# Performance work log

Measured on AMD Instinct MI355X. Metric: run time of the kernel, lower is better.

## Reference

```python
import jax, jax.numpy as jnp
import numpy as np

D_MODEL = 1024
N_HEADS = 16
HEAD_DIM = D_MODEL // N_HEADS


def setup_inputs() -> dict:
    key = jax.random.key(0)
    k1, k2, k3 = jax.random.split(key, 3)
    B, T = 4, 2048
    x = jax.random.normal(k1, (B, T, D_MODEL), dtype=jnp.float32)
    # match nn.Linear default init scale roughly (small weights for stability)
    w_qkv = jax.random.normal(k2, (D_MODEL, 3 * D_MODEL), dtype=jnp.float32) / np.sqrt(D_MODEL)
    w_proj = jax.random.normal(k3, (D_MODEL, D_MODEL), dtype=jnp.float32) / np.sqrt(D_MODEL)
    b_proj = jnp.zeros((D_MODEL,), dtype=jnp.float32)
    return {"x": x, "w_qkv": w_qkv, "w_proj": w_proj, "b_proj": b_proj}


def reference(x, w_qkv, w_proj, b_proj):
    B, T, C = x.shape
    qkv = x @ w_qkv  # [B,T,3C]
    q, k, v = jnp.split(qkv, 3, axis=-1)
    # [B, H, T, hd]
    q = q.reshape(B, T, N_HEADS, HEAD_DIM).transpose(0, 2, 1, 3)
    k = k.reshape(B, T, N_HEADS, HEAD_DIM).transpose(0, 2, 1, 3)
    v = v.reshape(B, T, N_HEADS, HEAD_DIM).transpose(0, 2, 1, 3)
    scale = 1.0 / np.sqrt(HEAD_DIM).astype(np.float32)
    att = jnp.einsum("bhqd,bhkd->bhqk", q, k) * scale
    causal = jnp.tril(jnp.ones((T, T), dtype=bool))
    att = jnp.where(causal[None, None], att, jnp.float32(-jnp.inf))
    att = jax.nn.softmax(att, axis=-1)
    # dropout p=0.0 (eval) -> identity
    out = jnp.einsum("bhqk,bhkd->bhqd", att, v)
    out = out.transpose(0, 2, 1, 3).reshape(B, T, C)
    return out @ w_proj + b_proj
```

## Files before the change

kernel.cpp:

```cpp
#include <hip/hip_runtime.h>
#include <stdint.h>

#define D_MODEL 1024
#define N_HEADS 16
#define HEAD_DIM 64
#define BATCH 4
#define SEQ 2048
#define ROWS (BATCH * SEQ)
#define K3 (3 * D_MODEL)
#define NQT (SEQ / 64)
#define SCALE_Q 0.1803368867f

typedef unsigned short u16;
typedef unsigned int u32;
typedef __attribute__((ext_vector_type(8))) short short8;
typedef __attribute__((ext_vector_type(4))) float floatx4;

typedef const __attribute__((address_space(1))) u32* gptr_t;
typedef __attribute__((address_space(3))) u32* lptr_t;

__device__ __forceinline__ unsigned cvt_pk(float lo, float hi) {
    unsigned r;
    asm("v_cvt_pk_bf16_f32 %0, %1, %2" : "=v"(r) : "v"(lo), "v"(hi));
    return r;
}

__global__ __launch_bounds__(256) void conv_f2b4(const float* __restrict__ x,
                                                 u16* __restrict__ xb, int n4) {
    int i = blockIdx.x * 256 + threadIdx.x;
    if (i < n4) {
        float4 v = ((const float4*)x)[i];
        uint2 p;
        p.x = cvt_pk(v.x, v.y);
        p.y = cvt_pk(v.z, v.w);
        ((uint2*)xb)[i] = p;
    }
}

__global__ __launch_bounds__(256) void transpose_f2b_t(const float* __restrict__ w,
                                                       u16* __restrict__ wt,
                                                       int R, int C) {
    __shared__ u16 tile[64][65];
    const int tx = threadIdx.x & 63;
    const int ty = threadIdx.x >> 6;
    const int r0 = blockIdx.y * 64, c0 = blockIdx.x * 64;
    #pragma unroll
    for (int i = 0; i < 16; i += 2) {
        const float a = w[(size_t)(r0 + i * 4 + ty) * C + c0 + tx];
        const float b = w[(size_t)(r0 + (i + 1) * 4 + ty) * C + c0 + tx];
        const unsigned p = cvt_pk(a, b);
        tile[i * 4 + ty][tx] = (u16)p;
        tile[(i + 1) * 4 + ty][tx] = (u16)(p >> 16);
    }
    __syncthreads();
    #pragma unroll
    for (int i = 0; i < 16; ++i) {
        const int c = i * 4 + ty;
        wt[(size_t)(c0 + c) * R + r0 + tx] = tile[tx][c];
    }
}

__global__ __launch_bounds__(256) void transpose_v2(const u16* __restrict__ v,
                                                    u16* __restrict__ vt) {
    __shared__ u16 tile[64][65];
    const int bh = blockIdx.y;
    const int t0 = blockIdx.x * 64;
    const int tx = threadIdx.x & 63, ty = threadIdx.x >> 6;
    const u16* src = v + ((size_t)bh * SEQ + t0) * HEAD_DIM;
    #pragma unroll
    for (int i = 0; i < 16; ++i) {
        const int r = i * 4 + ty;
        tile[r][tx] = src[r * HEAD_DIM + tx];
    }
    __syncthreads();
    u16* dst = vt + (size_t)bh * HEAD_DIM * SEQ + t0;
    #pragma unroll
    for (int i = 0; i < 16; ++i) {
        const int d = i * 4 + ty;
        dst[(size_t)d * SEQ + tx] = tile[tx][d];
    }
}

#define GEMM_CORE_GLD(KDIM, NXB)                                               \
    __shared__ u16 As[128][64];                                                \
    __shared__ u16 Bs[128][64];                                                \
    const int tid  = threadIdx.x;                                              \
    const int wave = tid >> 6, lane = tid & 63;                                \
    const int quad = lane >> 4, l15 = lane & 15;                               \
    const int wr = wave >> 1, wc = wave & 1;                                   \
    const int bid = (int)(blockIdx.y * gridDim.x + blockIdx.x);                \
    const int nwg = (int)(gridDim.x * gridDim.y);                              \
    const int swz = (bid & 7) * (nwg >> 3) + (bid >> 3);      \
    const int m0 = (swz / (NXB)) * 128, n0 = (swz % (NXB)) * 128;              \
    const int lrow8 = lane >> 3;                                               \
    const int csw = 8 * ((lane & 7) ^ lrow8);           \
    const int swA = (l15 & 7) * 8;                      \
    floatx4 acc[4][4] = {};                                                    \
    for (int k0 = 0; k0 < (KDIM); k0 += 64) {                                  \
        _Pragma("unroll")                                                      \
        for (int i = 0; i < 4; ++i) {                                          \
            const int rb = i * 32 + wave * 8;                                  \
            const int r  = rb + lrow8;                                         \
            __builtin_amdgcn_global_load_lds(                                  \
                (gptr_t)(A + (size_t)(m0 + r) * (KDIM) + k0 + csw),            \
                (lptr_t)(&As[rb][0]), 16, 0, 0);                               \
            __builtin_amdgcn_global_load_lds(                                  \
                (gptr_t)(Bt + (size_t)(n0 + r) * (KDIM) + k0 + csw),           \
                (lptr_t)(&Bs[rb][0]), 16, 0, 0);                               \
        }                                                                      \
        __syncthreads();                                                       \
        _Pragma("unroll")                                                      \
        for (int ks = 0; ks < 2; ++ks) {                                       \
            const int kk = ks * 32 + quad * 8;                                 \
            short8 af[4], bf[4];                                               \
            _Pragma("unroll")                                                  \
            for (int t = 0; t < 4; ++t) {                                      \
                af[t] = *(const short8*)&As[wr * 64 + t * 16 + l15][kk ^ swA]; \
                bf[t] = *(const short8*)&Bs[wc * 64 + t * 16 + l15][kk ^ swA]; \
            }                                                                  \
            _Pragma("unroll")                                                  \
            for (int i = 0; i < 4; ++i)                                        \
                _Pragma("unroll")                                              \
                for (int j = 0; j < 4; ++j)                                    \
                    acc[i][j] = __builtin_amdgcn_mfma_f32_16x16x32_bf16(       \
                        af[i], bf[j], acc[i][j], 0, 0, 0);                     \
        }                                                                      \
        __syncthreads();                                                       \
    }

__global__ __launch_bounds__(256) void gemm_qkv(const u16* __restrict__ A,
                                                const u16* __restrict__ Bt,
                                                u16* __restrict__ qo,
                                                u16* __restrict__ ko,
                                                u16* __restrict__ vo) {
    GEMM_CORE_GLD(D_MODEL, 24)
    const int which = n0 >> 10;
    u16* dst = which == 0 ? qo : (which == 1 ? ko : vo);
    const float scl = which == 0 ? SCALE_Q : 1.f;
    #pragma unroll
    for (int i = 0; i < 4; ++i)
        #pragma unroll
        for (int j = 0; j < 4; ++j) {
            const int col = n0 + wc * 64 + j * 16 + l15;
            const int rb  = m0 + wr * 64 + i * 16 + quad * 4;
            const int cc  = col & 1023;
            const int h = cc >> 6, d = cc & 63;
            #pragma unroll
            for (int rr = 0; rr < 4; rr += 2) {
                const unsigned pw = cvt_pk(acc[i][j][rr] * scl,
                                           acc[i][j][rr + 1] * scl);
                int row = rb + rr;
                int b_ = row >> 11, t_ = row & 2047;
                dst[(((size_t)(b_ * N_HEADS + h)) * SEQ + t_) * HEAD_DIM + d] =
                    (u16)pw;
                row = rb + rr + 1;
                b_ = row >> 11; t_ = row & 2047;
                dst[(((size_t)(b_ * N_HEADS + h)) * SEQ + t_) * HEAD_DIM + d] =
                    (u16)(pw >> 16);
            }
        }
}

__global__ __launch_bounds__(256) void gemm_proj(const u16* __restrict__ A,
                                                 const u16* __restrict__ Bt,
                                                 const float* __restrict__ bias,
                                                 float* __restrict__ out) {
    GEMM_CORE_GLD(D_MODEL, 8)
    #pragma unroll
    for (int i = 0; i < 4; ++i)
        #pragma unroll
        for (int j = 0; j < 4; ++j) {
            const int col = n0 + wc * 64 + j * 16 + l15;
            const int rb  = m0 + wr * 64 + i * 16 + quad * 4;
            const float bv = bias[col];
            #pragma unroll
            for (int rr = 0; rr < 4; ++rr) {
                const int row = rb + rr;
                out[(size_t)row * D_MODEL + col] = acc[i][j][rr] + bv;
            }
        }
}

__global__ __launch_bounds__(256, 4) void attn_mfma(const u16* __restrict__ q,
                                                    const u16* __restrict__ k,
                                                    const u16* __restrict__ vt,
                                                    u16* __restrict__ o) {
    __shared__ u16 Ks[2][64][64];
    __shared__ u16 Vs[2][64][64];
    __shared__ u16 Plds[4][16][64];
    const int tid = threadIdx.x;
    const int w = tid >> 6, lane = tid & 63;
    const int quad = lane >> 4, l15 = lane & 15;
    const int bid = (int)(blockIdx.y * 16 + blockIdx.x);
    const int swzb = (bid & 7) * 128 + (bid >> 3);
    const int bh = swzb >> 4;
    const int qx = swzb & 15;
    const int b = bh >> 4, h = bh & 15;
    const u16* kb  = k  + (size_t)bh * SEQ * HEAD_DIM;
    const u16* vtb = vt + (size_t)bh * HEAD_DIM * SEQ;
    const int lrow8 = lane >> 3;
    const int csw = 8 * ((lane & 7) ^ lrow8);
    const int swA = (l15 & 7) * 8;
    const int r0 = w * 16 + lrow8;
    const short8 ones = {0x3F80, 0x3F80, 0x3F80, 0x3F80,
                         0x3F80, 0x3F80, 0x3F80, 0x3F80};

    #pragma unroll 1
    for (int seg = 0; seg < 2; ++seg) {
        const int qt = seg ? qx : (NQT - 1 - qx);
        const int qrow = qt * 64 + w * 16 + l15;
        const u16* qp = q + ((size_t)bh * SEQ + qrow) * HEAD_DIM + quad * 8;
        const short8 bq0 = *(const short8*)(qp);
        const short8 bq1 = *(const short8*)(qp + 32);

        floatx4 O[4] = {};
        floatx4 Lacc = {};

        __syncthreads();
        __builtin_amdgcn_global_load_lds(
            (gptr_t)(kb + (size_t)(r0) * HEAD_DIM + csw),
            (lptr_t)(&Ks[0][w * 16][0]), 16, 0, 0);
        __builtin_amdgcn_global_load_lds(
            (gptr_t)(kb + (size_t)(r0 + 8) * HEAD_DIM + csw),
            (lptr_t)(&Ks[0][w * 16 + 8][0]), 16, 0, 0);
        __builtin_amdgcn_global_load_lds(
            (gptr_t)(vtb + (size_t)(r0) * SEQ + csw),
            (lptr_t)(&Vs[0][w * 16][0]), 16, 0, 0);
        __builtin_amdgcn_global_load_lds(
            (gptr_t)(vtb + (size_t)(r0 + 8) * SEQ + csw),
            (lptr_t)(&Vs[0][w * 16 + 8][0]), 16, 0, 0);

        for (int c = 0; c <= qt; ++c) {
            const int cb = c & 1;
            __syncthreads();
            if (c < qt) {
                const int nb = cb ^ 1;
                __builtin_amdgcn_global_load_lds(
                    (gptr_t)(kb + (size_t)((c + 1) * 64 + r0) * HEAD_DIM + csw),
                    (lptr_t)(&Ks[nb][w * 16][0]), 16, 0, 0);
                __builtin_amdgcn_global_load_lds(
                    (gptr_t)(kb + (size_t)((c + 1) * 64 + r0 + 8) * HEAD_DIM + csw),
                    (lptr_t)(&Ks[nb][w * 16 + 8][0]), 16, 0, 0);
                __builtin_amdgcn_global_load_lds(
                    (gptr_t)(vtb + (size_t)(r0) * SEQ + (c + 1) * 64 + csw),
                    (lptr_t)(&Vs[nb][w * 16][0]), 16, 0, 0);
                __builtin_amdgcn_global_load_lds(
                    (gptr_t)(vtb + (size_t)(r0 + 8) * SEQ + (c + 1) * 64 + csw),
                    (lptr_t)(&Vs[nb][w * 16 + 8][0]), 16, 0, 0);
            }
            floatx4 s[4];
            #pragma unroll
            for (int kt = 0; kt < 4; ++kt) {
                short8 ak0 = *(const short8*)&Ks[cb][kt * 16 + l15][(quad * 8) ^ swA];
                short8 ak1 = *(const short8*)&Ks[cb][kt * 16 + l15][(32 + quad * 8) ^ swA];
                floatx4 z = {};
                z = __builtin_amdgcn_mfma_f32_16x16x32_bf16(ak0, bq0, z, 0, 0, 0);
                z = __builtin_amdgcn_mfma_f32_16x16x32_bf16(ak1, bq1, z, 0, 0, 0);
                s[kt] = z;
            }
            float e[4][4];
            #pragma unroll
            for (int kt = 0; kt < 4; ++kt)
                #pragma unroll
                for (int r = 0; r < 4; ++r)
                    e[kt][r] = exp2f(s[kt][r]);
            if (c == qt) {
                #pragma unroll
                for (int kt = 0; kt < 4; ++kt)
                    #pragma unroll
                    for (int r = 0; r < 4; ++r)
                        if (kt * 16 + quad * 4 + r > w * 16 + l15) e[kt][r] = 0.f;
            }
            #pragma unroll
            for (int kt = 0; kt < 4; ++kt) {
                uint2 pkv;
                pkv.x = cvt_pk(e[kt][0], e[kt][1]);
                pkv.y = cvt_pk(e[kt][2], e[kt][3]);
                *(uint2*)&Plds[w][l15][(kt * 16 + quad * 4) ^ swA] = pkv;
            }
            short8 pb0 = *(const short8*)&Plds[w][l15][(quad * 8) ^ swA];
            short8 pb1 = *(const short8*)&Plds[w][l15][(32 + quad * 8) ^ swA];
            #pragma unroll
            for (int dt = 0; dt < 4; ++dt) {
                short8 av0 = *(const short8*)&Vs[cb][dt * 16 + l15][(quad * 8) ^ swA];
                short8 av1 = *(const short8*)&Vs[cb][dt * 16 + l15][(32 + quad * 8) ^ swA];
                O[dt] = __builtin_amdgcn_mfma_f32_16x16x32_bf16(av0, pb0, O[dt], 0, 0, 0);
                O[dt] = __builtin_amdgcn_mfma_f32_16x16x32_bf16(av1, pb1, O[dt], 0, 0, 0);
            }
            Lacc = __builtin_amdgcn_mfma_f32_16x16x32_bf16(ones, pb0, Lacc, 0, 0, 0);
            Lacc = __builtin_amdgcn_mfma_f32_16x16x32_bf16(ones, pb1, Lacc, 0, 0, 0);
        }
        const float inv = 1.f / Lacc[0];
        u16* op = o + ((size_t)(b * SEQ + qrow)) * D_MODEL + h * 64 + quad * 4;
        #pragma unroll
        for (int dt = 0; dt < 4; ++dt) {
            uint2 pkv;
            pkv.x = cvt_pk(O[dt][0] * inv, O[dt][1] * inv);
            pkv.y = cvt_pk(O[dt][2] * inv, O[dt][3] * inv);
            *(uint2*)(op + dt * 16) = pkv;
        }
    }
}

extern "C" void kernel_launch(void* const* d_in, const int* in_sizes, int n_in,
                              void* d_out, int out_size, void* d_ws, size_t ws_size,
                              hipStream_t stream) {
    const float* x      = (const float*)d_in[0];
    const float* w_qkv  = (const float*)d_in[1];
    const float* w_proj = (const float*)d_in[2];
    const float* b_proj = (const float*)d_in[3];
    float* out = (float*)d_out;

    u16* xb      = (u16*)d_ws;
    u16* wt_qkv  = xb + (size_t)ROWS * D_MODEL;
    u16* wt_proj = wt_qkv + (size_t)D_MODEL * K3;
    u16* qws     = wt_proj + (size_t)D_MODEL * D_MODEL;
    u16* kws     = qws + (size_t)ROWS * D_MODEL;
    u16* vtws    = kws + (size_t)ROWS * D_MODEL;
    u16* aout    = vtws + (size_t)ROWS * D_MODEL;
    u16* vnat    = aout;

    conv_f2b4<<<(ROWS * D_MODEL / 4 + 255) / 256, 256, 0, stream>>>(x, xb, ROWS * D_MODEL / 4);
    transpose_f2b_t<<<dim3(K3 / 64, D_MODEL / 64), 256, 0, stream>>>(w_qkv, wt_qkv, D_MODEL, K3);
    transpose_f2b_t<<<dim3(D_MODEL / 64, D_MODEL / 64), 256, 0, stream>>>(w_proj, wt_proj, D_MODEL, D_MODEL);

    gemm_qkv<<<dim3(K3 / 128, ROWS / 128), 256, 0, stream>>>(xb, wt_qkv, qws, kws, vnat);

    transpose_v2<<<dim3(SEQ / 64, BATCH * N_HEADS), 256, 0, stream>>>(vnat, vtws);

    attn_mfma<<<dim3(NQT / 2, BATCH * N_HEADS), 256, 0, stream>>>(qws, kws, vtws, aout);

    gemm_proj<<<dim3(D_MODEL / 128, ROWS / 128), 256, 0, stream>>>(aout, wt_proj, b_proj, out);
}
```

Baseline: 254.6 us.

## Feed P to PV MFMA directly from registers via 16x16x16 bf16 instructions

Removes the per-wave LDS round trip for the probability tile. The score-MFMA output layout already matches the B-operand layout of the 16x16x16 bf16 MFMA, so each 4-element packed block is fed in directly. V reads become 8-byte LDS loads and the PV step now issues twice as many MFMA instructions. The change also adds s_setprio around the MFMA groups and raises the launch-bounds occupancy hint from 4 to 5 blocks per CU, which may cause register spills. If the builtin is missing, an inline-asm fallback pads with s_nops, which would be slow.

```diff
diff --git a/kernel.cpp b/kernel.cpp
--- a/kernel.cpp
+++ b/kernel.cpp
@@ -14,7 +14,9 @@
 typedef unsigned short u16;
 typedef unsigned int u32;
 typedef __attribute__((ext_vector_type(8))) short short8;
+typedef __attribute__((ext_vector_type(4))) short short4b;
 typedef __attribute__((ext_vector_type(4))) float floatx4;
+typedef __attribute__((ext_vector_type(2))) unsigned int uint2v;
 
 typedef const __attribute__((address_space(1))) u32* gptr_t;
 typedef __attribute__((address_space(3))) u32* lptr_t;
@@ -24,6 +26,30 @@
     asm("v_cvt_pk_bf16_f32 %0, %1, %2" : "=v"(r) : "v"(lo), "v"(hi));
     return r;
 }
+
+__device__ __forceinline__ short4b pack4(float a, float b, float c, float d) {
+    uint2v t;
+    t.x = cvt_pk(a, b);
+    t.y = cvt_pk(c, d);
+    return __builtin_bit_cast(short4b, t);
+}
+
+#if defined(__has_builtin)
+#if __has_builtin(__builtin_amdgcn_mfma_f32_16x16x16bf16_1k)
+#define MFMA16(a, b, c) __builtin_amdgcn_mfma_f32_16x16x16bf16_1k(a, b, c, 0, 0, 0)
+#endif
+#endif
+#ifndef MFMA16
+__device__ __forceinline__ floatx4 mfma16_asm(short4b a, short4b b, floatx4 c) {
+    asm volatile("s_nop 1\n\t"
+                 "v_mfma_f32_16x16x16_bf16 %0, %1, %2, %0\n\t"
+                 "s_nop 7\n\t"
+                 "s_nop 7"
+                 : "+v"(c) : "v"(a), "v"(b));
+    return c;
+}
+#define MFMA16(a, b, c) mfma16_asm(a, b, c)
+#endif
 
 __global__ __launch_bounds__(256) void conv_f2b4(const float* __restrict__ x,
                                                  u16* __restrict__ xb, int n4) {
@@ -181,13 +207,12 @@
         }
 }
 
-__global__ __launch_bounds__(256, 4) void attn_mfma(const u16* __restrict__ q,
+__global__ __launch_bounds__(256, 5) void attn_mfma(const u16* __restrict__ q,
                                                     const u16* __restrict__ k,
                                                     const u16* __restrict__ vt,
                                                     u16* __restrict__ o) {
     __shared__ u16 Ks[2][64][64];
     __shared__ u16 Vs[2][64][64];
-    __shared__ u16 Plds[4][16][64];
     const int tid = threadIdx.x;
     const int w = tid >> 6, lane = tid & 63;
     const int quad = lane >> 4, l15 = lane & 15;
@@ -202,8 +227,7 @@
     const int csw = 8 * ((lane & 7) ^ lrow8);
     const int swA = (l15 & 7) * 8;
     const int r0 = w * 16 + lrow8;
-    const short8 ones = {0x3F80, 0x3F80, 0x3F80, 0x3F80,
-                         0x3F80, 0x3F80, 0x3F80, 0x3F80};
+    const short4b ones4 = {0x3F80, 0x3F80, 0x3F80, 0x3F80};
 
     #pragma unroll 1
     for (int seg = 0; seg < 2; ++seg) {
@@ -254,8 +278,10 @@
                 short8 ak0 = *(const short8*)&Ks[cb][kt * 16 + l15][(quad * 8) ^ swA];
                 short8 ak1 = *(const short8*)&Ks[cb][kt * 16 + l15][(32 + quad * 8) ^ swA];
                 floatx4 z = {};
+                __builtin_amdgcn_s_setprio(1);
                 z = __builtin_amdgcn_mfma_f32_16x16x32_bf16(ak0, bq0, z, 0, 0, 0);
                 z = __builtin_amdgcn_mfma_f32_16x16x32_bf16(ak1, bq1, z, 0, 0, 0);
+                __builtin_amdgcn_s_setprio(0);
                 s[kt] = z;
             }
             float e[4][4];
@@ -271,24 +297,24 @@
                     for (int r = 0; r < 4; ++r)
                         if (kt * 16 + quad * 4 + r > w * 16 + l15) e[kt][r] = 0.f;
             }
-            #pragma unroll
-            for (int kt = 0; kt < 4; ++kt) {
-                uint2 pkv;
-                pkv.x = cvt_pk(e[kt][0], e[kt][1]);
-                pkv.y = cvt_pk(e[kt][2], e[kt][3]);
-                *(uint2*)&Plds[w][l15][(kt * 16 + quad * 4) ^ swA] = pkv;
-            }
-            short8 pb0 = *(const short8*)&Plds[w][l15][(quad * 8) ^ swA];
-            short8 pb1 = *(const short8*)&Plds[w][l15][(32 + quad * 8) ^ swA];
+            short4b pb[4];
+            #pragma unroll
+            for (int kt = 0; kt < 4; ++kt)
+                pb[kt] = pack4(e[kt][0], e[kt][1], e[kt][2], e[kt][3]);
+            __builtin_amdgcn_s_setprio(1);
             #pragma unroll
             for (int dt = 0; dt < 4; ++dt) {
-                short8 av0 = *(const short8*)&Vs[cb][dt * 16 + l15][(quad * 8) ^ swA];
-                short8 av1 = *(const short8*)&Vs[cb][dt * 16 + l15][(32 + quad * 8) ^ swA];
-                O[dt] = __builtin_amdgcn_mfma_f32_16x16x32_bf16(av0, pb0, O[dt], 0, 0, 0);
-                O[dt] = __builtin_amdgcn_mfma_f32_16x16x32_bf16(av1, pb1, O[dt], 0, 0, 0);
-            }
-            Lacc = __builtin_amdgcn_mfma_f32_16x16x32_bf16(ones, pb0, Lacc, 0, 0, 0);
-            Lacc = __builtin_amdgcn_mfma_f32_16x16x32_bf16(ones, pb1, Lacc, 0, 0, 0);
+                #pragma unroll
+                for (int kt = 0; kt < 4; ++kt) {
+                    const short4b av = *(const short4b*)
+                        &Vs[cb][dt * 16 + l15][(kt * 16 + quad * 4) ^ swA];
+                    O[dt] = MFMA16(av, pb[kt], O[dt]);
+                }
+            }
+            #pragma unroll
+            for (int kt = 0; kt < 4; ++kt)
+                Lacc = MFMA16(ones4, pb[kt], Lacc);
+            __builtin_amdgcn_s_setprio(0);
         }
         const float inv = 1.f / Lacc[0];
         u16* op = o + ((size_t)(b * SEQ + qrow)) * D_MODEL + h * 64 + quad * 4;
```

New measurement: 260.6 us. +2.3%, slower.
